# Performance work log

Measured on AMD Instinct MI355X. Metric: run time of the kernel, lower is better.

The kernel has to match this reference:

```python
import jax, jax.numpy as jnp
import numpy as np

DIM = 256
HEADS = 8
BALL = 128          # ball_size m
DIMENSIONALITY = 3
HIDDEN = 4 * DIM    # mlp_ratio * dim
HEAD_DIM = DIM // HEADS
EPS = 1e-6


def setup_inputs() -> dict:
    key = jax.random.key(0)
    ks = jax.random.split(key, 16)
    N = 131072
    s = lambda *sh: 1.0 / np.sqrt(sh[-1])
    inp = {
        "x": jax.random.normal(ks[0], (N, DIM), jnp.float32),
        "pos": jax.random.normal(ks[1], (N, DIMENSIONALITY), jnp.float32),
        "num_batches": 8,
        # BallMSA params
        "qkv_w": jax.random.normal(ks[2], (3 * DIM, DIM), jnp.float32) * s(DIM),
        "qkv_b": jnp.zeros((3 * DIM,), jnp.float32),
        "proj_w": jax.random.normal(ks[3], (DIM, DIM), jnp.float32) * s(DIM),
        "proj_b": jnp.zeros((DIM,), jnp.float32),
        "pe_w": jax.random.normal(ks[4], (DIM, DIMENSIONALITY), jnp.float32) * s(DIMENSIONALITY),
        "pe_b": jnp.zeros((DIM,), jnp.float32),
        "sigma_att": -1.0 + 0.01 * jax.random.normal(ks[5], (1, HEADS, 1, 1), jnp.float32),
        # norms
        "norm1_w": jnp.ones((DIM,), jnp.float32),
        "norm2_w": jnp.ones((DIM,), jnp.float32),
        # SwiGLU MLP
        "w1_w": jax.random.normal(ks[6], (HIDDEN, DIM), jnp.float32) * s(DIM),
        "w1_b": jnp.zeros((HIDDEN,), jnp.float32),
        "w2_w": jax.random.normal(ks[7], (HIDDEN, DIM), jnp.float32) * s(DIM),
        "w2_b": jnp.zeros((HIDDEN,), jnp.float32),
        "w3_w": jax.random.normal(ks[8], (DIM, HIDDEN), jnp.float32) * s(HIDDEN),
        "w3_b": jnp.zeros((DIM,), jnp.float32),
    }
    return inp


def _rmsnorm(x, w):
    return x * jax.lax.rsqrt(jnp.mean(x * x, axis=-1, keepdims=True) + EPS) * w


def _ball_msa(x, pos, qkv_w, qkv_b, proj_w, proj_b, pe_w, pe_b, sigma_att):
    N = x.shape[0]
    n = N // BALL
    p = pos.reshape(n, BALL, DIMENSIONALITY)
    # relative position wrt ball center (eq. 9), torch.no_grad in original
    rel = jax.lax.stop_gradient((p - p.mean(axis=1, keepdims=True)).reshape(N, DIMENSIONALITY))
    x = x + rel @ pe_w.T + pe_b
    # qkv: last dim laid out as (H E K) with K innermost
    qkv = (x @ qkv_w.T + qkv_b).reshape(n, BALL, HEADS, HEAD_DIM, 3)
    q = jnp.transpose(qkv[..., 0], (0, 2, 1, 3))  # n H m E
    k = jnp.transpose(qkv[..., 1], (0, 2, 1, 3))
    v = jnp.transpose(qkv[..., 2], (0, 2, 1, 3))
    # distance-based bias (eq. 10), torch.no_grad in original
    d = jnp.sqrt(jnp.sum((p[:, :, None, :] - p[:, None, :, :]) ** 2, axis=-1))  # n m m
    bias = jax.lax.stop_gradient(sigma_att[0]) * jax.lax.stop_gradient(d)[:, None, :, :]  # n H m m
    scores = jnp.einsum('nhme,nhke->nhmk', q, k) / np.sqrt(HEAD_DIM) + bias
    attn = jax.nn.softmax(scores, axis=-1)
    out = jnp.einsum('nhmk,nhke->nhme', attn, v)
    out = jnp.transpose(out, (0, 2, 1, 3)).reshape(N, DIM)  # (n m) (H E)
    return out @ proj_w.T + proj_b


def reference(x, pos, num_batches, qkv_w, qkv_b, proj_w, proj_b, pe_w, pe_b,
              sigma_att, norm1_w, norm2_w, w1_w, w1_b, w2_w, w2_b, w3_w, w3_b):
    # pre-norm block: x + BMSA(norm1(x)); x + SwiGLU(norm2(x))
    x = x + _ball_msa(_rmsnorm(x, norm1_w), pos, qkv_w, qkv_b, proj_w, proj_b,
                      pe_w, pe_b, sigma_att)
    h = _rmsnorm(x, norm2_w)
    gate = jax.nn.silu(h @ w1_w.T + w1_b)
    val = h @ w2_w.T + w2_b
    return x + (gate * val) @ w3_w.T + w3_b
```

## Files before the change

### kernel.cpp

```cpp
#include <hip/hip_runtime.h>

typedef __bf16 bf16x8 __attribute__((ext_vector_type(8)));
typedef float f32x4 __attribute__((ext_vector_type(4)));

__device__ __forceinline__ float b2f(unsigned short u) {
    union { unsigned int i; float f; } v; v.i = ((unsigned int)u) << 16; return v.f;
}
__device__ __forceinline__ unsigned short f2b(float f) {
    union { float f; unsigned int i; } v; v.f = f;
    unsigned int r = (v.i + 0x7fffu + ((v.i >> 16) & 1u)) >> 16;
    return (unsigned short)r;
}

__device__ __forceinline__ void gload16(const void* g, void* l) {
    __builtin_amdgcn_global_load_lds(
        (const __attribute__((address_space(1))) unsigned int*)g,
        (__attribute__((address_space(3))) unsigned int*)l,
        16, 0, 0);
}

__global__ __launch_bounds__(256)
void k_cvt5(const float* __restrict__ s0, const float* __restrict__ s1,
            const float* __restrict__ s2, const float* __restrict__ s3,
            const float* __restrict__ s4, unsigned short* __restrict__ dst)
{
    size_t gid = ((size_t)blockIdx.x * 256 + threadIdx.x) * 4;
    const float* src; size_t off;
    if      (gid < 196608) { src = s0; off = 0; }
    else if (gid < 262144) { src = s1; off = 196608; }
    else if (gid < 524288) { src = s2; off = 262144; }
    else if (gid < 786432) { src = s3; off = 524288; }
    else                   { src = s4; off = 786432; }
    float4 v = *(const float4*)(src + (gid - off));
    uint2 pk;
    pk.x = (unsigned int)f2b(v.x) | ((unsigned int)f2b(v.y) << 16);
    pk.y = (unsigned int)f2b(v.z) | ((unsigned int)f2b(v.w) << 16);
    *(uint2*)(dst + gid) = pk;
}

__global__ __launch_bounds__(256)
void k_norm1_pe(const float* __restrict__ x,
                const float* __restrict__ pos,
                const float* __restrict__ n1w,
                const float* __restrict__ pew,
                const float* __restrict__ peb,
                unsigned short* __restrict__ out)
{
    __shared__ float spw0[256], spw1[256], spw2[256], speb[256], snw[256];
    __shared__ float px[128], py[128], pz[128];
    __shared__ float mean[3];
    const int tid = threadIdx.x;
    const int ball = blockIdx.x;

    spw0[tid] = pew[tid*3+0]; spw1[tid] = pew[tid*3+1]; spw2[tid] = pew[tid*3+2];
    speb[tid] = peb[tid];     snw[tid]  = n1w[tid];
    if (tid < 128) {
        const float* pp = pos + (size_t)(ball*128 + tid)*3;
        px[tid] = pp[0]; py[tid] = pp[1]; pz[tid] = pp[2];
    }
    __syncthreads();
    if (tid < 3) {
        const float* arr = (tid==0) ? px : (tid==1) ? py : pz;
        float s = 0.f;
        for (int i = 0; i < 128; ++i) s += arr[i];
        mean[tid] = s * (1.0f/128.0f);
    }
    __syncthreads();

    const int wave = tid >> 6, lane = tid & 63;
    const float m0 = mean[0], m1 = mean[1], m2 = mean[2];
    for (int tok = wave; tok < 128; tok += 4) {
        size_t row = (size_t)(ball*128 + tok);
        float4 xv = *(const float4*)(x + row*256 + lane*4);
        float xf[4] = { xv.x, xv.y, xv.z, xv.w };
        float ss = xf[0]*xf[0] + xf[1]*xf[1] + xf[2]*xf[2] + xf[3]*xf[3];
        #pragma unroll
        for (int off = 1; off < 64; off <<= 1) ss += __shfl_xor(ss, off);
        float rstd = rsqrtf(ss * (1.0f/256.0f) + 1e-6f);
        float r0 = px[tok] - m0, r1 = py[tok] - m1, r2 = pz[tok] - m2;
        unsigned short o[4];
        #pragma unroll
        for (int k = 0; k < 4; ++k) {
            int j = lane*4 + k;
            float hv = xf[k] * rstd * snw[j];
            o[k] = f2b(hv + r0*spw0[j] + r1*spw1[j] + r2*spw2[j] + speb[j]);
        }
        uint2 pk;
        pk.x = (unsigned int)o[0] | ((unsigned int)o[1] << 16);
        pk.y = (unsigned int)o[2] | ((unsigned int)o[3] << 16);
        *(uint2*)(out + row*256 + lane*4) = pk;
    }
}

__global__ __launch_bounds__(256)
void k_rmsnorm(const float* __restrict__ x,
               const float* __restrict__ w,
               unsigned short* __restrict__ out)
{
    const int lane = threadIdx.x & 63;
    const size_t token = (size_t)blockIdx.x*4 + (threadIdx.x >> 6);
    float4 xv = *(const float4*)(x + token*256 + lane*4);
    float xf[4] = { xv.x, xv.y, xv.z, xv.w };
    float ss = xf[0]*xf[0] + xf[1]*xf[1] + xf[2]*xf[2] + xf[3]*xf[3];
    #pragma unroll
    for (int off = 1; off < 64; off <<= 1) ss += __shfl_xor(ss, off);
    float rstd = rsqrtf(ss * (1.0f/256.0f) + 1e-6f);
    float4 wv = *(const float4*)(w + lane*4);
    unsigned short o[4] = { f2b(xf[0]*rstd*wv.x), f2b(xf[1]*rstd*wv.y),
                            f2b(xf[2]*rstd*wv.z), f2b(xf[3]*rstd*wv.w) };
    uint2 pk;
    pk.x = (unsigned int)o[0] | ((unsigned int)o[1] << 16);
    pk.y = (unsigned int)o[2] | ((unsigned int)o[3] << 16);
    *(uint2*)(out + token*256 + lane*4) = pk;
}

__device__ __forceinline__ void gemm_mainloop_bt(
    const unsigned short* __restrict__ A, const unsigned short* __restrict__ B,
    int K, int m0, int n0, int tid,
    unsigned short* sA, unsigned short* sB, f32x4 (&acc)[4][4])
{
    const int lane = tid & 63, lane16 = lane & 15, quad = lane >> 4;
    const int wave = tid >> 6;
    const int wm = (wave >> 1) * 64, wn = (wave & 1) * 64;
    const int srow = wave * 32 + (lane >> 2);
    const int scol = (lane & 3) * 8;
    const unsigned short* pA = A + (size_t)(m0 + srow) * K + scol;
    const unsigned short* pB = B + (size_t)(n0 + srow) * K + scol;
    const size_t row16 = (size_t)16 * K;
    unsigned short* lA = sA + wave * 1024;
    unsigned short* lB = sB + wave * 1024;

    for (int k0 = 0; k0 < K; k0 += 32) {
        __syncthreads();
        gload16(pA + k0,         lA);
        gload16(pA + row16 + k0, lA + 512);
        gload16(pB + k0,         lB);
        gload16(pB + row16 + k0, lB + 512);
        __syncthreads();
        bf16x8 af[4], bfr[4];
        #pragma unroll
        for (int i = 0; i < 4; ++i) af[i]  = *(const bf16x8*)&sA[(wm + i*16 + lane16)*32 + quad*8];
        #pragma unroll
        for (int j = 0; j < 4; ++j) bfr[j] = *(const bf16x8*)&sB[(wn + j*16 + lane16)*32 + quad*8];
        #pragma unroll
        for (int i = 0; i < 4; ++i)
            #pragma unroll
            for (int j = 0; j < 4; ++j)
                acc[i][j] = __builtin_amdgcn_mfma_f32_16x16x32_bf16(af[i], bfr[j], acc[i][j], 0, 0, 0);
    }
}

__global__ __launch_bounds__(256, 2)
void k_gemm_bias(const unsigned short* __restrict__ A,
                 const unsigned short* __restrict__ B,
                 const float* __restrict__ bias,
                 const float* residual,
                 void* C, int K, int Ncols, int outBf16)
{
    __shared__ __align__(16) unsigned short sA[128*32];
    __shared__ __align__(16) unsigned short sB[128*32];
    const int tid = threadIdx.x;
    const int m0 = blockIdx.x * 128, n0 = blockIdx.y * 128;
    f32x4 zero = {0.f, 0.f, 0.f, 0.f};
    f32x4 acc[4][4];
    #pragma unroll
    for (int i = 0; i < 4; ++i)
        #pragma unroll
        for (int j = 0; j < 4; ++j) acc[i][j] = zero;

    gemm_mainloop_bt(A, B, K, m0, n0, tid, sA, sB, acc);

    const int lane = tid & 63, lane16 = lane & 15, quad = lane >> 4;
    const int wave = tid >> 6, wm = (wave >> 1) * 64, wn = (wave & 1) * 64;
    #pragma unroll
    for (int i = 0; i < 4; ++i)
        #pragma unroll
        for (int j = 0; j < 4; ++j) {
            int n = n0 + wn + j*16 + lane16;
            float bj = bias[n];
            #pragma unroll
            for (int r = 0; r < 4; ++r) {
                int m = m0 + wm + i*16 + quad*4 + r;
                size_t idx = (size_t)m * Ncols + n;
                float v = acc[i][j][r] + bj;
                if (residual) v += residual[idx];
                if (outBf16) ((unsigned short*)C)[idx] = f2b(v);
                else         ((float*)C)[idx] = v;
            }
        }
}

__global__ __launch_bounds__(256, 2)
void k_gemm_swiglu(const unsigned short* __restrict__ A,
                   const unsigned short* __restrict__ B1,
                   const unsigned short* __restrict__ B2,
                   const float* __restrict__ b1,
                   const float* __restrict__ b2,
                   unsigned short* __restrict__ C, int K)
{
    __shared__ __align__(16) unsigned short sA[128*32];
    __shared__ __align__(16) unsigned short sB1[128*32];
    __shared__ __align__(16) unsigned short sB2[128*32];
    const int tid = threadIdx.x;
    const int m0 = blockIdx.x * 128, n0 = blockIdx.y * 128;
    const int lane = tid & 63, lane16 = lane & 15, quad = lane >> 4;
    const int wave = tid >> 6, wm = (wave >> 1) * 64, wn = (wave & 1) * 64;
    const int srow = wave * 32 + (lane >> 2);
    const int scol = (lane & 3) * 8;
    const unsigned short* pA  = A  + (size_t)(m0 + srow) * K + scol;
    const unsigned short* pB1 = B1 + (size_t)(n0 + srow) * K + scol;
    const unsigned short* pB2 = B2 + (size_t)(n0 + srow) * K + scol;
    const size_t row16 = (size_t)16 * K;
    unsigned short* lA  = sA  + wave * 1024;
    unsigned short* lB1g = sB1 + wave * 1024;
    unsigned short* lB2g = sB2 + wave * 1024;

    f32x4 zero = {0.f, 0.f, 0.f, 0.f};
    f32x4 accg[4][4], accv[4][4];
    #pragma unroll
    for (int i = 0; i < 4; ++i)
        #pragma unroll
        for (int j = 0; j < 4; ++j) { accg[i][j] = zero; accv[i][j] = zero; }

    for (int k0 = 0; k0 < K; k0 += 32) {
        __syncthreads();
        gload16(pA  + k0,         lA);
        gload16(pA  + row16 + k0, lA + 512);
        gload16(pB1 + k0,         lB1g);
        gload16(pB1 + row16 + k0, lB1g + 512);
        gload16(pB2 + k0,         lB2g);
        gload16(pB2 + row16 + k0, lB2g + 512);
        __syncthreads();
        bf16x8 af[4], bg[4], bv[4];
        #pragma unroll
        for (int i = 0; i < 4; ++i) af[i] = *(const bf16x8*)&sA[(wm + i*16 + lane16)*32 + quad*8];
        #pragma unroll
        for (int j = 0; j < 4; ++j) {
            bg[j] = *(const bf16x8*)&sB1[(wn + j*16 + lane16)*32 + quad*8];
            bv[j] = *(const bf16x8*)&sB2[(wn + j*16 + lane16)*32 + quad*8];
        }
        #pragma unroll
        for (int i = 0; i < 4; ++i)
            #pragma unroll
            for (int j = 0; j < 4; ++j) {
                accg[i][j] = __builtin_amdgcn_mfma_f32_16x16x32_bf16(af[i], bg[j], accg[i][j], 0, 0, 0);
                accv[i][j] = __builtin_amdgcn_mfma_f32_16x16x32_bf16(af[i], bv[j], accv[i][j], 0, 0, 0);
            }
    }

    #pragma unroll
    for (int i = 0; i < 4; ++i)
        #pragma unroll
        for (int j = 0; j < 4; ++j) {
            int n = n0 + wn + j*16 + lane16;
            float bjg = b1[n], bjv = b2[n];
            #pragma unroll
            for (int r = 0; r < 4; ++r) {
                int m = m0 + wm + i*16 + quad*4 + r;
                float g  = accg[i][j][r] + bjg;
                float vv = accv[i][j][r] + bjv;
                float sg = 1.0f / (1.0f + __expf(-g));
                C[(size_t)m * 1024 + n] = f2b(g * sg * vv);
            }
        }
}

__global__ __launch_bounds__(256, 2)
void k_attn(const unsigned short* __restrict__ qkv,
            const float* __restrict__ pos,
            const float* __restrict__ sigma,
            unsigned short* __restrict__ out)
{
    __shared__ __align__(16) unsigned short Qs[128*40];
    __shared__ __align__(16) unsigned short Ks[128*40];
    __shared__ __align__(16) unsigned short Vt[32*136];
    __shared__ __align__(16) unsigned short Ps[128*136];
    __shared__ float px[128], py[128], pz[128];

    const int ball = blockIdx.x >> 3;
    const int h    = blockIdx.x & 7;
    const int tid  = threadIdx.x;

    {
        int tok = tid >> 1;
        int e0  = (tid & 1) * 16;
        const unsigned short* rowp = qkv + (size_t)(ball*128 + tok)*768 + h*96 + e0*3;
        unsigned short u[48];
        #pragma unroll
        for (int c = 0; c < 6; ++c) *(uint4*)&u[c*8] = *(const uint4*)(rowp + c*8);
        #pragma unroll
        for (int e = 0; e < 16; ++e) {
            Qs[tok*40 + e0 + e]    = u[e*3 + 0];
            Ks[tok*40 + e0 + e]    = u[e*3 + 1];
            Vt[(e0 + e)*136 + tok] = u[e*3 + 2];
        }
    }
    if (tid < 128) {
        const float* pp = pos + (size_t)(ball*128 + tid)*3;
        px[tid] = pp[0]; py[tid] = pp[1]; pz[tid] = pp[2];
    }
    __syncthreads();

    const int wave = tid >> 6, lane = tid & 63, lane16 = lane & 15, quad = lane >> 4;
    const float sig = sigma[h];
    const float scale = 0.17677669529663687f;
    f32x4 zero = {0.f, 0.f, 0.f, 0.f};

    f32x4 s[2][8];
    {
        bf16x8 a[2];
        #pragma unroll
        for (int i = 0; i < 2; ++i)
            a[i] = *(const bf16x8*)&Qs[(wave*32 + i*16 + lane16)*40 + quad*8];
        #pragma unroll
        for (int j = 0; j < 8; ++j) {
            bf16x8 b = *(const bf16x8*)&Ks[(j*16 + lane16)*40 + quad*8];
            #pragma unroll
            for (int i = 0; i < 2; ++i)
                s[i][j] = __builtin_amdgcn_mfma_f32_16x16x32_bf16(a[i], b, zero, 0, 0, 0);
        }
    }

    float pnx[8], pny[8], pnz[8];
    #pragma unroll
    for (int j = 0; j < 8; ++j) {
        int n = j*16 + lane16;
        pnx[j] = px[n]; pny[j] = py[n]; pnz[j] = pz[n];
    }
    float l[2][4];
    #pragma unroll
    for (int i = 0; i < 2; ++i)
        #pragma unroll
        for (int r = 0; r < 4; ++r) {
            int m = wave*32 + i*16 + quad*4 + r;
            float pmx = px[m], pmy = py[m], pmz = pz[m];
            float sv[8];
            float mx = -1e30f;
            #pragma unroll
            for (int j = 0; j < 8; ++j) {
                float dx = pmx - pnx[j], dy = pmy - pny[j], dz = pmz - pnz[j];
                float d = sqrtf(dx*dx + dy*dy + dz*dz);
                float val = s[i][j][r] * scale + sig * d;
                sv[j] = val;
                mx = fmaxf(mx, val);
            }
            #pragma unroll
            for (int off = 1; off < 16; off <<= 1) mx = fmaxf(mx, __shfl_xor(mx, off, 16));
            float sum = 0.f;
            #pragma unroll
            for (int j = 0; j < 8; ++j) {
                float p = __expf(sv[j] - mx);
                sum += p;
                Ps[(size_t)m*136 + j*16 + lane16] = f2b(p);
            }
            #pragma unroll
            for (int off = 1; off < 16; off <<= 1) sum += __shfl_xor(sum, off, 16);
            l[i][r] = sum;
        }
    __syncthreads();

    f32x4 o[2][2];
    #pragma unroll
    for (int i = 0; i < 2; ++i)
        #pragma unroll
        for (int nf = 0; nf < 2; ++nf) o[i][nf] = zero;
    #pragma unroll
    for (int c = 0; c < 4; ++c) {
        bf16x8 pa[2];
        #pragma unroll
        for (int i = 0; i < 2; ++i)
            pa[i] = *(const bf16x8*)&Ps[(wave*32 + i*16 + lane16)*136 + c*32 + quad*8];
        #pragma unroll
        for (int nf = 0; nf < 2; ++nf) {
            bf16x8 vb = *(const bf16x8*)&Vt[(nf*16 + lane16)*136 + c*32 + quad*8];
            #pragma unroll
            for (int i = 0; i < 2; ++i)
                o[i][nf] = __builtin_amdgcn_mfma_f32_16x16x32_bf16(pa[i], vb, o[i][nf], 0, 0, 0);
        }
    }

    #pragma unroll
    for (int i = 0; i < 2; ++i)
        #pragma unroll
        for (int nf = 0; nf < 2; ++nf)
            #pragma unroll
            for (int r = 0; r < 4; ++r) {
                int m = wave*32 + i*16 + quad*4 + r;
                out[(size_t)(ball*128 + m)*256 + h*32 + nf*16 + lane16] = f2b(o[i][nf][r] / l[i][r]);
            }
}

extern "C" void kernel_launch(void* const* d_in, const int* in_sizes, int n_in,
                              void* d_out, int out_size, void* d_ws, size_t ws_size,
                              hipStream_t stream)
{
    const float* x      = (const float*)d_in[0];
    const float* pos    = (const float*)d_in[1];
    const float* qkv_w  = (const float*)d_in[3];
    const float* qkv_b  = (const float*)d_in[4];
    const float* proj_w = (const float*)d_in[5];
    const float* proj_b = (const float*)d_in[6];
    const float* pe_w   = (const float*)d_in[7];
    const float* pe_b   = (const float*)d_in[8];
    const float* sigma  = (const float*)d_in[9];
    const float* n1w    = (const float*)d_in[10];
    const float* n2w    = (const float*)d_in[11];
    const float* w1w    = (const float*)d_in[12];
    const float* w1b    = (const float*)d_in[13];
    const float* w2w    = (const float*)d_in[14];
    const float* w2b    = (const float*)d_in[15];
    const float* w3w    = (const float*)d_in[16];
    const float* w3b    = (const float*)d_in[17];

    const int N = in_sizes[0] / 256;
    float* out = (float*)d_out;

    unsigned short* wb      = (unsigned short*)d_ws;
    unsigned short* qkv_wb  = wb;
    unsigned short* proj_wb = wb + 196608;
    unsigned short* w1wb    = wb + 262144;
    unsigned short* w2wb    = wb + 524288;
    unsigned short* w3wb    = wb + 786432;

    int C = 1;
    while (2097152 + (size_t)(N / C) * 2560 > ws_size && C < 256) C <<= 1;
    const int R = N / C;
    unsigned short* regA = wb + 1048576;
    unsigned short* regB = regA + (size_t)R * 1024;

    k_cvt5<<<1024, 256, 0, stream>>>(qkv_w, proj_w, w1w, w2w, w3w, wb);

    for (int c = 0; c < C; ++c) {
        const size_t row0 = (size_t)c * R;
        const float* x_c   = x   + row0 * 256;
        const float* pos_c = pos + row0 * 3;
        float* out_c = out + row0 * 256;
        const int nball_c = R / 128;

        k_norm1_pe<<<nball_c, 256, 0, stream>>>(x_c, pos_c, n1w, pe_w, pe_b, regB);
        k_gemm_bias<<<dim3(R/128, 6), 256, 0, stream>>>(regB, qkv_wb, qkv_b, nullptr, regA, 256, 768, 1);
        k_attn<<<nball_c * 8, 256, 0, stream>>>(regA, pos_c, sigma, regB);
        k_gemm_bias<<<dim3(R/128, 2), 256, 0, stream>>>(regB, proj_wb, proj_b, x_c, out_c, 256, 256, 0);
        k_rmsnorm<<<R/4, 256, 0, stream>>>(out_c, n2w, regB);
        k_gemm_swiglu<<<dim3(R/128, 8), 256, 0, stream>>>(regB, w1wb, w2wb, w1b, w2b, regA, 256);
        k_gemm_bias<<<dim3(R/128, 2), 256, 0, stream>>>(regA, w3wb, w3b, out_c, out_c, 1024, 256, 0);
    }
}
```

Before: 1.142 ms.

## Remap blocks for XCD locality and shrink SwiGLU N-tile to raise occupancy

Adds an XCD-aware block index remap so that consecutive blocks on the same XCD share A rows. This is meant to improve L2 reuse across the chiplets, and it is applied to the GEMM and attention kernels, which now use 1D grids. The SwiGLU GEMM N-tile shrinks from 128 to 64, which halves the accumulator registers and LDS so three blocks fit per CU. The cost is that A tiles are reloaded twice as often.

```diff
diff --git a/kernel.cpp b/kernel.cpp
--- a/kernel.cpp
+++ b/kernel.cpp
@@ -17,6 +17,19 @@
         (const __attribute__((address_space(1))) unsigned int*)g,
         (__attribute__((address_space(3))) unsigned int*)l,
         16, 0, 0);
+}
+
+__device__ __forceinline__ void xcd_map(int bid, int nx, int ny, int& bx, int& by) {
+    if ((nx & 7) == 0) {
+        int xcd = bid & 7;
+        int s   = bid >> 3;
+        int xl  = s / ny;
+        by = s - xl * ny;
+        bx = xcd * (nx >> 3) + xl;
+    } else {
+        bx = bid / ny;
+        by = bid - bx * ny;
+    }
 }
 
 __global__ __launch_bounds__(256)
@@ -155,12 +168,14 @@
                  const unsigned short* __restrict__ B,
                  const float* __restrict__ bias,
                  const float* residual,
-                 void* C, int K, int Ncols, int outBf16)
+                 void* C, int K, int Ncols, int outBf16, int ny)
 {
     __shared__ __align__(16) unsigned short sA[128*32];
     __shared__ __align__(16) unsigned short sB[128*32];
     const int tid = threadIdx.x;
-    const int m0 = blockIdx.x * 128, n0 = blockIdx.y * 128;
+    int bx, by;
+    xcd_map(blockIdx.x, gridDim.x / ny, ny, bx, by);
+    const int m0 = bx * 128, n0 = by * 128;
     f32x4 zero = {0.f, 0.f, 0.f, 0.f};
     f32x4 acc[4][4];
     #pragma unroll
@@ -190,59 +205,61 @@
         }
 }
 
-__global__ __launch_bounds__(256, 2)
+__global__ __launch_bounds__(256, 3)
 void k_gemm_swiglu(const unsigned short* __restrict__ A,
                    const unsigned short* __restrict__ B1,
                    const unsigned short* __restrict__ B2,
                    const float* __restrict__ b1,
                    const float* __restrict__ b2,
-                   unsigned short* __restrict__ C, int K)
+                   unsigned short* __restrict__ C, int K, int ny)
 {
     __shared__ __align__(16) unsigned short sA[128*32];
-    __shared__ __align__(16) unsigned short sB1[128*32];
-    __shared__ __align__(16) unsigned short sB2[128*32];
+    __shared__ __align__(16) unsigned short sB1[64*32];
+    __shared__ __align__(16) unsigned short sB2[64*32];
     const int tid = threadIdx.x;
-    const int m0 = blockIdx.x * 128, n0 = blockIdx.y * 128;
+    int bx, by;
+    xcd_map(blockIdx.x, gridDim.x / ny, ny, bx, by);
+    const int m0 = bx * 128, n0 = by * 64;
     const int lane = tid & 63, lane16 = lane & 15, quad = lane >> 4;
-    const int wave = tid >> 6, wm = (wave >> 1) * 64, wn = (wave & 1) * 64;
-    const int srow = wave * 32 + (lane >> 2);
-    const int scol = (lane & 3) * 8;
-    const unsigned short* pA  = A  + (size_t)(m0 + srow) * K + scol;
-    const unsigned short* pB1 = B1 + (size_t)(n0 + srow) * K + scol;
-    const unsigned short* pB2 = B2 + (size_t)(n0 + srow) * K + scol;
+    const int wave = tid >> 6;
+    const int wm = (wave >> 1) * 64, wn = (wave & 1) * 32;
+    const int srowA = wave * 32 + (lane >> 2);
+    const int srowB = wave * 16 + (lane >> 2);
+    const int scol  = (lane & 3) * 8;
+    const unsigned short* pA  = A  + (size_t)(m0 + srowA) * K + scol;
+    const unsigned short* pB1 = B1 + (size_t)(n0 + srowB) * K + scol;
+    const unsigned short* pB2 = B2 + (size_t)(n0 + srowB) * K + scol;
     const size_t row16 = (size_t)16 * K;
     unsigned short* lA  = sA  + wave * 1024;
-    unsigned short* lB1g = sB1 + wave * 1024;
-    unsigned short* lB2g = sB2 + wave * 1024;
+    unsigned short* lB1 = sB1 + wave * 512;
+    unsigned short* lB2 = sB2 + wave * 512;
 
     f32x4 zero = {0.f, 0.f, 0.f, 0.f};
-    f32x4 accg[4][4], accv[4][4];
+    f32x4 accg[4][2], accv[4][2];
     #pragma unroll
     for (int i = 0; i < 4; ++i)
         #pragma unroll
-        for (int j = 0; j < 4; ++j) { accg[i][j] = zero; accv[i][j] = zero; }
+        for (int j = 0; j < 2; ++j) { accg[i][j] = zero; accv[i][j] = zero; }
 
     for (int k0 = 0; k0 < K; k0 += 32) {
         __syncthreads();
-        gload16(pA  + k0,         lA);
-        gload16(pA  + row16 + k0, lA + 512);
-        gload16(pB1 + k0,         lB1g);
-        gload16(pB1 + row16 + k0, lB1g + 512);
-        gload16(pB2 + k0,         lB2g);
-        gload16(pB2 + row16 + k0, lB2g + 512);
+        gload16(pA + k0,         lA);
+        gload16(pA + row16 + k0, lA + 512);
+        gload16(pB1 + k0,        lB1);
+        gload16(pB2 + k0,        lB2);
         __syncthreads();
-        bf16x8 af[4], bg[4], bv[4];
+        bf16x8 af[4], bg[2], bv[2];
         #pragma unroll
         for (int i = 0; i < 4; ++i) af[i] = *(const bf16x8*)&sA[(wm + i*16 + lane16)*32 + quad*8];
         #pragma unroll
-        for (int j = 0; j < 4; ++j) {
+        for (int j = 0; j < 2; ++j) {
             bg[j] = *(const bf16x8*)&sB1[(wn + j*16 + lane16)*32 + quad*8];
             bv[j] = *(const bf16x8*)&sB2[(wn + j*16 + lane16)*32 + quad*8];
         }
         #pragma unroll
         for (int i = 0; i < 4; ++i)
             #pragma unroll
-            for (int j = 0; j < 4; ++j) {
+            for (int j = 0; j < 2; ++j) {
                 accg[i][j] = __builtin_amdgcn_mfma_f32_16x16x32_bf16(af[i], bg[j], accg[i][j], 0, 0, 0);
                 accv[i][j] = __builtin_amdgcn_mfma_f32_16x16x32_bf16(af[i], bv[j], accv[i][j], 0, 0, 0);
             }
@@ -251,7 +268,7 @@
     #pragma unroll
     for (int i = 0; i < 4; ++i)
         #pragma unroll
-        for (int j = 0; j < 4; ++j) {
+        for (int j = 0; j < 2; ++j) {
             int n = n0 + wn + j*16 + lane16;
             float bjg = b1[n], bjv = b2[n];
             #pragma unroll
@@ -277,8 +294,8 @@
     __shared__ __align__(16) unsigned short Ps[128*136];
     __shared__ float px[128], py[128], pz[128];
 
-    const int ball = blockIdx.x >> 3;
-    const int h    = blockIdx.x & 7;
+    int ball, h;
+    xcd_map(blockIdx.x, gridDim.x >> 3, 8, ball, h);
     const int tid  = threadIdx.x;
 
     {
@@ -436,13 +453,14 @@
         const float* pos_c = pos + row0 * 3;
         float* out_c = out + row0 * 256;
         const int nball_c = R / 128;
+        const int nx = R / 128;
 
         k_norm1_pe<<<nball_c, 256, 0, stream>>>(x_c, pos_c, n1w, pe_w, pe_b, regB);
-        k_gemm_bias<<<dim3(R/128, 6), 256, 0, stream>>>(regB, qkv_wb, qkv_b, nullptr, regA, 256, 768, 1);
+        k_gemm_bias<<<nx * 6, 256, 0, stream>>>(regB, qkv_wb, qkv_b, nullptr, regA, 256, 768, 1, 6);
         k_attn<<<nball_c * 8, 256, 0, stream>>>(regA, pos_c, sigma, regB);
-        k_gemm_bias<<<dim3(R/128, 2), 256, 0, stream>>>(regB, proj_wb, proj_b, x_c, out_c, 256, 256, 0);
+        k_gemm_bias<<<nx * 2, 256, 0, stream>>>(regB, proj_wb, proj_b, x_c, out_c, 256, 256, 0, 2);
         k_rmsnorm<<<R/4, 256, 0, stream>>>(out_c, n2w, regB);
-        k_gemm_swiglu<<<dim3(R/128, 8), 256, 0, stream>>>(regB, w1wb, w2wb, w1b, w2b, regA, 256);
-        k_gemm_bias<<<dim3(R/128, 2), 256, 0, stream>>>(regA, w3wb, w3b, out_c, out_c, 1024, 256, 0);
-    }
-}
+        k_gemm_swiglu<<<nx * 16, 256, 0, stream>>>(regB, w1wb, w2wb, w1b, w2b, regA, 256, 16);
+        k_gemm_bias<<<nx * 2, 256, 0, stream>>>(regA, w3wb, w3b, out_c, out_c, 1024, 256, 0, 2);
+    }
+}
```

Result: faster. 1.076 ms (-5.8%).
